# Kernel optimization log

Hardware: AMD Instinct MI355X
Metric: run time of the kernel (lower is better)

## Reference

```python
import jax, jax.numpy as jnp
import numpy as np

EPS = 1e-05
K = 32


def _knn_idx(xyz_B3N, k):
    # negative squared pairwise distance: -||xi||^2 + 2 xi.xj - ||xj||^2
    inner = 2.0 * jnp.einsum('bdn,bdm->bnm', xyz_B3N, xyz_B3N)  # [B,N,N]
    xx = jnp.sum(xyz_B3N ** 2, axis=1)  # [B,N]
    pd = inner - xx[:, :, None] - xx[:, None, :]
    _, idx = jax.lax.top_k(pd, k)  # [B,N,k] nearest (largest negative dist)
    return idx


def setup_inputs() -> dict:
    key = jax.random.key(0)
    k1, k2 = jax.random.split(key)
    B, N, C = 16, 4096, 64
    xyz_B3N = jax.random.normal(k1, (B, 3, N), dtype=jnp.float32)
    feats_BNC = jax.random.normal(k2, (B, N, C), dtype=jnp.float32)
    alpha = jnp.ones((C,), dtype=jnp.float32)
    beta = jnp.zeros((C,), dtype=jnp.float32)
    return {"xyz_B3N": xyz_B3N, "feats_BNC": feats_BNC, "alpha": alpha, "beta": beta}


def reference(xyz_B3N, feats_BNC, alpha, beta):
    idx = _knn_idx(xyz_B3N, K)  # [B,N,k]
    # gather neighbor features directly: [B,N,k,C]
    neigh = jax.vmap(lambda f, i: f[i])(feats_BNC, idx)
    offset = neigh - feats_BNC[:, :, None, :]  # [B,N,k,C]
    sigma = jnp.mean(offset ** 2)  # global scalar
    gaed = (offset / (sigma + EPS)) * alpha + beta
    pooled = jnp.max(gaed, axis=2)  # [B,N,C]
    return pooled
```

## Files before the change

### kernel.cpp

```cpp
#include <hip/hip_runtime.h>
#include <float.h>

#define BB 16
#define NN 4096
#define CC 64
#define KNN 32
#define NSLICE 16
#define SSZ 256
#define CKEEP 8
#define NQ 65536


__device__ __forceinline__ int lane_rank(unsigned long long m) {
    return __builtin_amdgcn_mbcnt_hi((unsigned)(m >> 32),
           __builtin_amdgcn_mbcnt_lo((unsigned)m, 0u));
}

__device__ __forceinline__ unsigned umaxu(unsigned a, unsigned b) {
    return a > b ? a : b;
}
__device__ __forceinline__ unsigned uminu(unsigned a, unsigned b) {
    return a < b ? a : b;
}
#define CE(a, b) { unsigned _mx = umaxu(a, b); b = uminu(a, b); a = _mx; }

__global__ __launch_bounds__(256) void prep_kernel(
        const float* __restrict__ xyz, float4* __restrict__ pts4,
        int* __restrict__ flag_cnt) {
#pragma clang fp contract(off)
    const int p = blockIdx.x * 256 + threadIdx.x;
    if (p == 0) flag_cnt[0] = 0;
    const int b = p >> 12;
    const int i = p & (NN - 1);
    const float* xb = xyz + (size_t)b * (3 * NN);
    float x = xb[i], y = xb[NN + i], z = xb[2 * NN + i];
    float xx = ((x * x) + (y * y)) + (z * z);
    pts4[p] = make_float4(x, y, z, xx);
}

__global__ __launch_bounds__(1024) void knn_select_kernel(
        const float4* __restrict__ pts4, unsigned* __restrict__ val_buf) {
#pragma clang fp contract(off)
    __shared__ float4 pts[SSZ];
    const int tid = threadIdx.x;
    const int blk = blockIdx.x;
    const int s = blk & 15;
    const int g2 = (blk >> 4) & 3;
    const int b = blk >> 6;
    const float4* pb = pts4 + (b << 12);

    if (tid < SSZ) pts[tid] = pb[(s << 8) | tid];
    const int q = (g2 << 10) | tid;
    const float4 qp = pb[q];
    const float qx = qp.x, qy = qp.y, qz = qp.z;
    const float nqxx = -qp.w;
    __syncthreads();

    unsigned h0=0,h1=0,h2=0,h3=0,h4=0,h5=0,h6=0,h7=0;
    const unsigned ibase = 4095u - (unsigned)(s << 8);

#define KY(ji, dst) { \
        float4 cp = pts[j0 + ji]; \
        float dot = __builtin_fmaf(qz, cp.z, \
                    __builtin_fmaf(qy, cp.y, qx * cp.x)); \
        float pd = __builtin_fmaf(2.0f, dot, nqxx) - cp.w; \
        pd = fminf(pd, 0.0f); \
        dst = (~__float_as_uint(pd) & 0xFFFFF000u) \
              | (ibase - (unsigned)(j0 + ji)); }

    for (int j0 = 0; j0 < SSZ; j0 += 8) {
        unsigned k0,k1,k2,k3,k4,k5,k6,k7;
        KY(0,k0) KY(1,k1) KY(2,k2) KY(3,k3)
        KY(4,k4) KY(5,k5) KY(6,k6) KY(7,k7)
        CE(k0,k1) CE(k2,k3) CE(k0,k2) CE(k1,k3) CE(k1,k2)
        CE(k4,k5) CE(k6,k7) CE(k4,k6) CE(k5,k7) CE(k5,k6)
        CE(k0,k4) CE(k1,k5) CE(k2,k6) CE(k3,k7)
        CE(k2,k4) CE(k3,k5)
        CE(k1,k2) CE(k3,k4) CE(k5,k6)
        h0 = umaxu(h0, k7); h1 = umaxu(h1, k6);
        h2 = umaxu(h2, k5); h3 = umaxu(h3, k4);
        h4 = umaxu(h4, k3); h5 = umaxu(h5, k2);
        h6 = umaxu(h6, k1); h7 = umaxu(h7, k0);
        CE(h0,h4) CE(h1,h5) CE(h2,h6) CE(h3,h7)
        CE(h0,h2) CE(h1,h3) CE(h4,h6) CE(h5,h7)
        CE(h0,h1) CE(h2,h3) CE(h4,h5) CE(h6,h7)
    }
#undef KY

    const int qg = (b << 12) | q;
    unsigned* vp = val_buf + (size_t)(s * CKEEP) * NQ + qg;
#define ST(t, ht) vp[(size_t)(t) * NQ] = ht;
    ST(0,h0) ST(1,h1) ST(2,h2) ST(3,h3)
    ST(4,h4) ST(5,h5) ST(6,h6) ST(7,h7)
#undef ST
}

__global__ __launch_bounds__(64) void knn_merge_kernel(
        const unsigned* __restrict__ val_buf, int* __restrict__ idx_out,
        int* __restrict__ flag_list, int* __restrict__ flag_cnt) {
    __shared__ unsigned lv[64 * 129];
    const int tid = threadIdx.x;
    const int qg = blockIdx.x * 64 + tid;
    unsigned* my = lv + tid * 129;
    for (int t = 0; t < 128; ++t) my[t] = val_buf[(size_t)t * NQ + qg];

    int p0=0,p1=0,p2=0,p3=0,p4=0,p5=0,p6=0,p7=0,
        p8=0,p9=0,p10=0,p11=0,p12=0,p13=0,p14=0,p15=0;
    unsigned v0 =my[0],  v1 =my[8],  v2 =my[16],  v3 =my[24];
    unsigned v4 =my[32], v5 =my[40], v6 =my[48],  v7 =my[56];
    unsigned v8 =my[64], v9 =my[72], v10=my[80],  v11=my[88];
    unsigned v12=my[96], v13=my[104],v14=my[112], v15=my[120];
    int* outp = idx_out + (size_t)qg * KNN;
    unsigned key32 = 0u, key33 = 0u;
    for (int step = 0; step < 33; ++step) {
        unsigned best = v0; int bp = 0;
        if (v1  > best) { best = v1;  bp = 1; }
        if (v2  > best) { best = v2;  bp = 2; }
        if (v3  > best) { best = v3;  bp = 3; }
        if (v4  > best) { best = v4;  bp = 4; }
        if (v5  > best) { best = v5;  bp = 5; }
        if (v6  > best) { best = v6;  bp = 6; }
        if (v7  > best) { best = v7;  bp = 7; }
        if (v8  > best) { best = v8;  bp = 8; }
        if (v9  > best) { best = v9;  bp = 9; }
        if (v10 > best) { best = v10; bp = 10; }
        if (v11 > best) { best = v11; bp = 11; }
        if (v12 > best) { best = v12; bp = 12; }
        if (v13 > best) { best = v13; bp = 13; }
        if (v14 > best) { best = v14; bp = 14; }
        if (v15 > best) { best = v15; bp = 15; }
        if (step == 32) { key33 = best; break; }
        outp[step] = 4095 - (int)(best & 4095u);
        if (step == 31) key32 = best;
        if      (bp==0)  { ++p0;  v0  = (p0 <8)?my[p0]      :0u; }
        else if (bp==1)  { ++p1;  v1  = (p1 <8)?my[8+p1]    :0u; }
        else if (bp==2)  { ++p2;  v2  = (p2 <8)?my[16+p2]   :0u; }
        else if (bp==3)  { ++p3;  v3  = (p3 <8)?my[24+p3]   :0u; }
        else if (bp==4)  { ++p4;  v4  = (p4 <8)?my[32+p4]   :0u; }
        else if (bp==5)  { ++p5;  v5  = (p5 <8)?my[40+p5]   :0u; }
        else if (bp==6)  { ++p6;  v6  = (p6 <8)?my[48+p6]   :0u; }
        else if (bp==7)  { ++p7;  v7  = (p7 <8)?my[56+p7]   :0u; }
        else if (bp==8)  { ++p8;  v8  = (p8 <8)?my[64+p8]   :0u; }
        else if (bp==9)  { ++p9;  v9  = (p9 <8)?my[72+p9]   :0u; }
        else if (bp==10) { ++p10; v10 = (p10<8)?my[80+p10]  :0u; }
        else if (bp==11) { ++p11; v11 = (p11<8)?my[88+p11]  :0u; }
        else if (bp==12) { ++p12; v12 = (p12<8)?my[96+p12]  :0u; }
        else if (bp==13) { ++p13; v13 = (p13<8)?my[104+p13] :0u; }
        else if (bp==14) { ++p14; v14 = (p14<8)?my[112+p14] :0u; }
        else             { ++p15; v15 = (p15<8)?my[120+p15] :0u; }
    }

    bool flag = ((key32 >> 12) == (key33 >> 12));
    for (int sl = 0; sl < 16; ++sl)
        flag = flag || (my[sl * 8 + 7] >= key33);
    if (flag) {
        int pos = atomicAdd(flag_cnt, 1);
        flag_list[pos] = qg;
    }
}

__global__ __launch_bounds__(256) void knn_fallback_kernel(
        const float* __restrict__ xyz, const int* __restrict__ flag_list,
        const int* __restrict__ flag_cnt, int* __restrict__ idx_out) {
#pragma clang fp contract(off)
    const int nflag = flag_cnt[0];
    const int lane = threadIdx.x & 63;
    const int wid = (blockIdx.x * 256 + threadIdx.x) >> 6;
    const int nw = (gridDim.x * 256) >> 6;
    for (int w = wid; w < nflag; w += nw) {
        const int qg = flag_list[w];
        const int b = qg >> 12;
        const int q = qg & (NN - 1);
        const float* xb = xyz + (size_t)b * (3 * NN);
        const float qx = xb[q], qy = xb[NN + q], qz = xb[2 * NN + q];
        const float qxx = ((qx * qx) + (qy * qy)) + (qz * qz);
        const float nqxx = -qxx;

        unsigned key[64];
#pragma unroll
        for (int i = 0; i < 64; ++i) {
            const int j = (i << 6) | lane;
            float x = xb[j], y = xb[NN + j], z = xb[2 * NN + j];
            float xxc = ((x * x) + (y * y)) + (z * z);
            float dot = __builtin_fmaf(qz, z, __builtin_fmaf(qy, y, qx * x));
            float pd = __builtin_fmaf(2.0f, dot, nqxx) - xxc;
            unsigned u = __float_as_uint(pd);
            key[i] = u ^ (unsigned)(((int)u >> 31) | 0x80000000);
        }

        unsigned cur = 0u;
        for (int bit = 31; bit >= 0; --bit) {
            const unsigned cand = cur | (1u << bit);
            int c = 0;
#pragma unroll
            for (int i = 0; i < 64; ++i) c += (key[i] >= cand) ? 1 : 0;
#pragma unroll
            for (int o = 32; o >= 1; o >>= 1) c += __shfl_xor(c, o, 64);
            if (c >= 32) cur = cand;
        }

        int ge = 0;
#pragma unroll
        for (int i = 0; i < 64; ++i) {
            ge += (key[i] > cur) ? 1 : 0;
            ge += (key[i] == cur) ? 0x10000 : 0;
        }
#pragma unroll
        for (int o = 32; o >= 1; o >>= 1) ge += __shfl_xor(ge, o, 64);
        const int gt_total = ge & 0xFFFF;
        const int budget = min(ge >> 16, 32 - gt_total);

        int* outp = idx_out + (size_t)qg * KNN;
        int slot = 0, neq = 0;
#pragma unroll
        for (int i = 0; i < 64; ++i) {
            const bool isgt = key[i] > cur;
            const bool iseq = key[i] == cur;
            const unsigned long long mgt = __ballot(isgt);
            const unsigned long long meq = __ballot(iseq);
            if (isgt) outp[slot + lane_rank(mgt)] = (i << 6) | lane;
            if (iseq) {
                const int r = neq + lane_rank(meq);
                if (r < budget) outp[gt_total + r] = (i << 6) | lane;
            }
            slot += __builtin_popcountll(mgt);
            neq += __builtin_popcountll(meq);
        }
    }
}

__global__ __launch_bounds__(256) void gather_minmax_kernel(
        const float* __restrict__ feats, const int* __restrict__ idx_in,
        float* __restrict__ mx_buf, float* __restrict__ mn_buf,
        double* __restrict__ partials) {
    const int tid = threadIdx.x;
    const int w = tid >> 6;
    const int lane = tid & 63;
    const int q = blockIdx.x * 4 + w;
    const int b = q >> 12;
    const float* fb = feats + (size_t)b * (NN * CC);
    const float center = feats[(size_t)q * CC + lane];
    const int* ip = idx_in + (size_t)q * KNN;

    float mx = -FLT_MAX, mn = FLT_MAX;
    double ss = 0.0;
#pragma unroll 4
    for (int k = 0; k < KNN; ++k) {
        int nb = ip[k];
        float v = fb[(size_t)nb * CC + lane];
        float off = v - center;
        mx = fmaxf(mx, off);
        mn = fminf(mn, off);
        double od = (double)off;
        ss = fma(od, od, ss);
    }
    mx_buf[(size_t)q * CC + lane] = mx;
    mn_buf[(size_t)q * CC + lane] = mn;

#pragma unroll
    for (int o = 32; o >= 1; o >>= 1) ss += __shfl_down(ss, o, 64);
    __shared__ double wsum[4];
    if (lane == 0) wsum[w] = ss;
    __syncthreads();
    if (tid == 0) partials[blockIdx.x] = (wsum[0] + wsum[1]) + (wsum[2] + wsum[3]);
}

__global__ __launch_bounds__(1024) void sigma_kernel(const double* __restrict__ partials,
                                                     float* __restrict__ sigma) {
    __shared__ double red[1024];
    double s = 0.0;
    for (int i = threadIdx.x; i < 16384; i += 1024) s += partials[i];
    red[threadIdx.x] = s;
    __syncthreads();
    for (int o = 512; o >= 1; o >>= 1) {
        if (threadIdx.x < o) red[threadIdx.x] += red[threadIdx.x + o];
        __syncthreads();
    }
    if (threadIdx.x == 0) sigma[0] = (float)(red[0] * (1.0 / 134217728.0));
}

__global__ __launch_bounds__(256) void finalize_kernel(
        const float* __restrict__ mx_buf, const float* __restrict__ mn_buf,
        const float* __restrict__ alpha, const float* __restrict__ beta,
        const float* __restrict__ sigma, float* __restrict__ out) {
#pragma clang fp contract(off)
    const int e = blockIdx.x * 256 + threadIdx.x;
    const int c = e & (CC - 1);
    const float s = sigma[0] + 1e-5f;
    const float a = alpha[c];
    const float bt = beta[c];
    const float off = (a >= 0.f) ? mx_buf[e] : mn_buf[e];
    const float t = off / s;
    out[e] = (t * a) + bt;
}

extern "C" void kernel_launch(void* const* d_in, const int* in_sizes, int n_in,
                              void* d_out, int out_size, void* d_ws, size_t ws_size,
                              hipStream_t stream) {
    (void)in_sizes; (void)n_in; (void)out_size; (void)ws_size;
    const float* xyz   = (const float*)d_in[0];
    const float* feats = (const float*)d_in[1];
    const float* alpha = (const float*)d_in[2];
    const float* beta  = (const float*)d_in[3];
    float* out = (float*)d_out;

    char* ws = (char*)d_ws;
    unsigned* val_buf  = (unsigned*)ws;
    float*    mx_buf   = (float*)ws;
    float*    mn_buf   = (float*)(ws + 16777216);
    int*      idx_buf  = (int*)(ws + 33554432);
    int*      flag_list= (int*)(ws + 41943040);
    int*      flag_cnt = (int*)(ws + 42205184);
    float4*   pts4     = (float4*)(ws + 42205248);
    double*   partials = (double*)(ws + 42205248);
    float*    sigma    = (float*)(ws + 43254784);

    prep_kernel<<<NQ / 256, 256, 0, stream>>>(xyz, pts4, flag_cnt);
    knn_select_kernel<<<BB * 4 * NSLICE, 1024, 0, stream>>>(pts4, val_buf);
    knn_merge_kernel<<<NQ / 64, 64, 0, stream>>>(val_buf, idx_buf,
                                                 flag_list, flag_cnt);
    knn_fallback_kernel<<<256, 256, 0, stream>>>(xyz, flag_list, flag_cnt,
                                                 idx_buf);
    gather_minmax_kernel<<<NQ / 4, 256, 0, stream>>>(feats, idx_buf, mx_buf,
                                                     mn_buf, partials);
    sigma_kernel<<<1, 1024, 0, stream>>>(partials, sigma);
    finalize_kernel<<<(NQ * CC) / 256, 256, 0, stream>>>(mx_buf, mn_buf, alpha,
                                                         beta, sigma, out);
}
```

Before: 342.5 us.

## Use packed FP32 math and two queries per thread in KNN select

Changes the point layout from float4 AoS to separate x/y/z/-norm arrays so each candidate pair loads as a float2. Distances are computed with v_pk_mul/v_pk_fma/v_pk_add inline asm, two candidates per instruction. Each thread now handles two queries against the same shared-memory slice, so every LDS load is reused twice. Blocks shrink to 256 threads and the grid doubles. The cost is more live registers, and the changed rounding order (2q precomputed, -xx added separately) may shift near-ties in the distance keys compared with before.

```diff
diff --git a/kernel.cpp b/kernel.cpp
--- a/kernel.cpp
+++ b/kernel.cpp
@@ -11,6 +11,8 @@
 #define NQ 65536
 
 
+typedef __attribute__((ext_vector_type(2))) float f32x2;
+
 __device__ __forceinline__ int lane_rank(unsigned long long m) {
     return __builtin_amdgcn_mbcnt_hi((unsigned)(m >> 32),
            __builtin_amdgcn_mbcnt_lo((unsigned)m, 0u));
@@ -24,9 +26,29 @@
 }
 #define CE(a, b) { unsigned _mx = umaxu(a, b); b = uminu(a, b); a = _mx; }
 
+__device__ __forceinline__ f32x2 pk_mul(f32x2 a, f32x2 b) {
+    f32x2 d;
+    asm("v_pk_mul_f32 %0, %1, %2" : "=v"(d) : "v"(a), "v"(b));
+    return d;
+}
+__device__ __forceinline__ f32x2 pk_fma(f32x2 a, f32x2 b, f32x2 c) {
+    f32x2 d;
+    asm("v_pk_fma_f32 %0, %1, %2, %3" : "=v"(d) : "v"(a), "v"(b), "v"(c));
+    return d;
+}
+__device__ __forceinline__ f32x2 pk_add(f32x2 a, f32x2 b) {
+    f32x2 d;
+    asm("v_pk_add_f32 %0, %1, %2" : "=v"(d) : "v"(a), "v"(b));
+    return d;
+}
+__device__ __forceinline__ f32x2 bc2(float s) {
+    f32x2 r; r[0] = s; r[1] = s; return r;
+}
+
 __global__ __launch_bounds__(256) void prep_kernel(
-        const float* __restrict__ xyz, float4* __restrict__ pts4,
-        int* __restrict__ flag_cnt) {
+        const float* __restrict__ xyz, float* __restrict__ gx,
+        float* __restrict__ gy, float* __restrict__ gz,
+        float* __restrict__ gn, int* __restrict__ flag_cnt) {
 #pragma clang fp contract(off)
     const int p = blockIdx.x * 256 + threadIdx.x;
     if (p == 0) flag_cnt[0] = 0;
@@ -35,63 +57,99 @@
     const float* xb = xyz + (size_t)b * (3 * NN);
     float x = xb[i], y = xb[NN + i], z = xb[2 * NN + i];
     float xx = ((x * x) + (y * y)) + (z * z);
-    pts4[p] = make_float4(x, y, z, xx);
-}
-
-__global__ __launch_bounds__(1024) void knn_select_kernel(
-        const float4* __restrict__ pts4, unsigned* __restrict__ val_buf) {
+    gx[p] = x; gy[p] = y; gz[p] = z; gn[p] = -xx;
+}
+
+__global__ __launch_bounds__(256) void knn_select_kernel(
+        const float* __restrict__ gx, const float* __restrict__ gy,
+        const float* __restrict__ gz, const float* __restrict__ gn,
+        unsigned* __restrict__ val_buf) {
 #pragma clang fp contract(off)
-    __shared__ float4 pts[SSZ];
+    __shared__ f32x2 lx2[128], ly2[128], lz2[128], ln2[128];
     const int tid = threadIdx.x;
     const int blk = blockIdx.x;
     const int s = blk & 15;
-    const int g2 = (blk >> 4) & 3;
-    const int b = blk >> 6;
-    const float4* pb = pts4 + (b << 12);
-
-    if (tid < SSZ) pts[tid] = pb[(s << 8) | tid];
-    const int q = (g2 << 10) | tid;
-    const float4 qp = pb[q];
-    const float qx = qp.x, qy = qp.y, qz = qp.z;
-    const float nqxx = -qp.w;
+    const int g8 = (blk >> 4) & 7;
+    const int b = blk >> 7;
+    const int pbase = (b << 12) | (s << 8);
+
+    ((float*)lx2)[tid] = gx[pbase + tid];
+    ((float*)ly2)[tid] = gy[pbase + tid];
+    ((float*)lz2)[tid] = gz[pbase + tid];
+    ((float*)ln2)[tid] = gn[pbase + tid];
+
+    const int q0 = (g8 << 9) | tid;
+    const int q1 = q0 + 256;
+    const int qb = b << 12;
+    const f32x2 Q2X0 = bc2(gx[qb + q0] + gx[qb + q0]);
+    const f32x2 Q2Y0 = bc2(gy[qb + q0] + gy[qb + q0]);
+    const f32x2 Q2Z0 = bc2(gz[qb + q0] + gz[qb + q0]);
+    const f32x2 NQX0 = bc2(gn[qb + q0]);
+    const f32x2 Q2X1 = bc2(gx[qb + q1] + gx[qb + q1]);
+    const f32x2 Q2Y1 = bc2(gy[qb + q1] + gy[qb + q1]);
+    const f32x2 Q2Z1 = bc2(gz[qb + q1] + gz[qb + q1]);
+    const f32x2 NQX1 = bc2(gn[qb + q1]);
     __syncthreads();
 
-    unsigned h0=0,h1=0,h2=0,h3=0,h4=0,h5=0,h6=0,h7=0;
+    unsigned ha0=0,ha1=0,ha2=0,ha3=0,ha4=0,ha5=0,ha6=0,ha7=0;
+    unsigned hb0=0,hb1=0,hb2=0,hb3=0,hb4=0,hb5=0,hb6=0,hb7=0;
     const unsigned ibase = 4095u - (unsigned)(s << 8);
 
-#define KY(ji, dst) { \
-        float4 cp = pts[j0 + ji]; \
-        float dot = __builtin_fmaf(qz, cp.z, \
-                    __builtin_fmaf(qy, cp.y, qx * cp.x)); \
-        float pd = __builtin_fmaf(2.0f, dot, nqxx) - cp.w; \
-        pd = fminf(pd, 0.0f); \
-        dst = (~__float_as_uint(pd) & 0xFFFFF000u) \
-              | (ibase - (unsigned)(j0 + ji)); }
-
-    for (int j0 = 0; j0 < SSZ; j0 += 8) {
-        unsigned k0,k1,k2,k3,k4,k5,k6,k7;
-        KY(0,k0) KY(1,k1) KY(2,k2) KY(3,k3)
-        KY(4,k4) KY(5,k5) KY(6,k6) KY(7,k7)
-        CE(k0,k1) CE(k2,k3) CE(k0,k2) CE(k1,k3) CE(k1,k2)
-        CE(k4,k5) CE(k6,k7) CE(k4,k6) CE(k5,k7) CE(k5,k6)
-        CE(k0,k4) CE(k1,k5) CE(k2,k6) CE(k3,k7)
-        CE(k2,k4) CE(k3,k5)
-        CE(k1,k2) CE(k3,k4) CE(k5,k6)
-        h0 = umaxu(h0, k7); h1 = umaxu(h1, k6);
-        h2 = umaxu(h2, k5); h3 = umaxu(h3, k4);
-        h4 = umaxu(h4, k3); h5 = umaxu(h5, k2);
-        h6 = umaxu(h6, k1); h7 = umaxu(h7, k0);
-        CE(h0,h4) CE(h1,h5) CE(h2,h6) CE(h3,h7)
-        CE(h0,h2) CE(h1,h3) CE(h4,h6) CE(h5,h7)
-        CE(h0,h1) CE(h2,h3) CE(h4,h5) CE(h6,h7)
-    }
-#undef KY
-
-    const int qg = (b << 12) | q;
-    unsigned* vp = val_buf + (size_t)(s * CKEEP) * NQ + qg;
-#define ST(t, ht) vp[(size_t)(t) * NQ] = ht;
-    ST(0,h0) ST(1,h1) ST(2,h2) ST(3,h3)
-    ST(4,h4) ST(5,h5) ST(6,h6) ST(7,h7)
+#define PDK(PX, PY, PZ, PN, QX, QY, QZ, NQX, JB, D0, D1) { \
+    f32x2 t = pk_mul(PX, QX); \
+    t = pk_fma(PY, QY, t); \
+    t = pk_fma(PZ, QZ, t); \
+    t = pk_add(t, NQX); \
+    t = pk_add(t, PN); \
+    float p0 = fminf(t[0], 0.0f), p1 = fminf(t[1], 0.0f); \
+    D0 = (~__float_as_uint(p0) & 0xFFFFF000u) | (ibase - (unsigned)(JB)); \
+    D1 = (~__float_as_uint(p1) & 0xFFFFF000u) | (ibase - (unsigned)(JB+1)); }
+
+#define NET8(HP) \
+    CE(k0,k1) CE(k2,k3) CE(k0,k2) CE(k1,k3) CE(k1,k2) \
+    CE(k4,k5) CE(k6,k7) CE(k4,k6) CE(k5,k7) CE(k5,k6) \
+    CE(k0,k4) CE(k1,k5) CE(k2,k6) CE(k3,k7) \
+    CE(k2,k4) CE(k3,k5) \
+    CE(k1,k2) CE(k3,k4) CE(k5,k6) \
+    HP##0 = umaxu(HP##0, k7); HP##1 = umaxu(HP##1, k6); \
+    HP##2 = umaxu(HP##2, k5); HP##3 = umaxu(HP##3, k4); \
+    HP##4 = umaxu(HP##4, k3); HP##5 = umaxu(HP##5, k2); \
+    HP##6 = umaxu(HP##6, k1); HP##7 = umaxu(HP##7, k0); \
+    CE(HP##0,HP##4) CE(HP##1,HP##5) CE(HP##2,HP##6) CE(HP##3,HP##7) \
+    CE(HP##0,HP##2) CE(HP##1,HP##3) CE(HP##4,HP##6) CE(HP##5,HP##7) \
+    CE(HP##0,HP##1) CE(HP##2,HP##3) CE(HP##4,HP##5) CE(HP##6,HP##7)
+
+    for (int j2 = 0; j2 < 128; j2 += 4) {
+        f32x2 xa = lx2[j2], xb2 = lx2[j2+1], xc = lx2[j2+2], xd = lx2[j2+3];
+        f32x2 ya = ly2[j2], yb = ly2[j2+1], yc = ly2[j2+2], yd = ly2[j2+3];
+        f32x2 za = lz2[j2], zb = lz2[j2+1], zc = lz2[j2+2], zd = lz2[j2+3];
+        f32x2 na = ln2[j2], nb = ln2[j2+1], nc = ln2[j2+2], nd = ln2[j2+3];
+        const int jb = j2 << 1;
+        {
+            unsigned k0,k1,k2,k3,k4,k5,k6,k7;
+            PDK(xa, ya, za, na, Q2X0, Q2Y0, Q2Z0, NQX0, jb+0, k0, k1)
+            PDK(xb2,yb, zb, nb, Q2X0, Q2Y0, Q2Z0, NQX0, jb+2, k2, k3)
+            PDK(xc, yc, zc, nc, Q2X0, Q2Y0, Q2Z0, NQX0, jb+4, k4, k5)
+            PDK(xd, yd, zd, nd, Q2X0, Q2Y0, Q2Z0, NQX0, jb+6, k6, k7)
+            NET8(ha)
+        }
+        {
+            unsigned k0,k1,k2,k3,k4,k5,k6,k7;
+            PDK(xa, ya, za, na, Q2X1, Q2Y1, Q2Z1, NQX1, jb+0, k0, k1)
+            PDK(xb2,yb, zb, nb, Q2X1, Q2Y1, Q2Z1, NQX1, jb+2, k2, k3)
+            PDK(xc, yc, zc, nc, Q2X1, Q2Y1, Q2Z1, NQX1, jb+4, k4, k5)
+            PDK(xd, yd, zd, nd, Q2X1, Q2Y1, Q2Z1, NQX1, jb+6, k6, k7)
+            NET8(hb)
+        }
+    }
+#undef PDK
+#undef NET8
+
+    unsigned* vp0 = val_buf + (size_t)(s * CKEEP) * NQ + (qb | q0);
+    unsigned* vp1 = val_buf + (size_t)(s * CKEEP) * NQ + (qb | q1);
+#define ST(t, p0v, p1v) { vp0[(size_t)(t) * NQ] = p0v; vp1[(size_t)(t) * NQ] = p1v; }
+    ST(0,ha0,hb0) ST(1,ha1,hb1) ST(2,ha2,hb2) ST(3,ha3,hb3)
+    ST(4,ha4,hb4) ST(5,ha5,hb5) ST(6,ha6,hb6) ST(7,ha7,hb7)
 #undef ST
 }
 
@@ -311,12 +369,16 @@
     int*      idx_buf  = (int*)(ws + 33554432);
     int*      flag_list= (int*)(ws + 41943040);
     int*      flag_cnt = (int*)(ws + 42205184);
-    float4*   pts4     = (float4*)(ws + 42205248);
+    float*    gx       = (float*)(ws + 42205248);
+    float*    gy       = (float*)(ws + 42467392);
+    float*    gz       = (float*)(ws + 42729536);
+    float*    gn       = (float*)(ws + 42991680);
     double*   partials = (double*)(ws + 42205248);
     float*    sigma    = (float*)(ws + 43254784);
 
-    prep_kernel<<<NQ / 256, 256, 0, stream>>>(xyz, pts4, flag_cnt);
-    knn_select_kernel<<<BB * 4 * NSLICE, 1024, 0, stream>>>(pts4, val_buf);
+    prep_kernel<<<NQ / 256, 256, 0, stream>>>(xyz, gx, gy, gz, gn, flag_cnt);
+    knn_select_kernel<<<BB * 8 * NSLICE, 256, 0, stream>>>(gx, gy, gz, gn,
+                                                           val_buf);
     knn_merge_kernel<<<NQ / 64, 64, 0, stream>>>(val_buf, idx_buf,
                                                  flag_list, flag_cnt);
     knn_fallback_kernel<<<256, 256, 0, stream>>>(xyz, flag_list, flag_cnt,
```

Result: slower. 365.1 us (+6.6%).
